# Kernel tuning notes

Hardware: AMD Instinct MI355X
Metric: run time of the kernel (lower is better)

The kernel has to match this reference:

```python
import jax, jax.numpy as jnp
import numpy as np

N_NODES = 50000
N_EDGES = 600000
D_EMB = 128
D_HID = 128
N_HEADS = 4
N_MABS = 7  # ISAB0(mab0,mab1), ISAB1(mab0,mab1), PMA, SAB, SAB
B, S = 16, 512
PROTO = 5


def setup_inputs() -> dict:
    key = jax.random.key(0)
    ks = jax.random.split(key, 24)
    nrm = lambda k, shape, s=0.05: jax.random.normal(k, shape, jnp.float32) * s
    node_embed = nrm(ks[0], (N_NODES + 1, D_EMB), 1.0).at[0].set(0.0)  # padding_idx=0
    return {
        'node_ids': jax.random.randint(ks[1], (B, S), 0, N_NODES),
        'edge_idx': jax.random.randint(ks[2], (2, N_EDGES), 0, N_NODES),
        'edge_attr': jax.random.normal(ks[3], (N_EDGES,), jnp.float32),
        'node_embed': node_embed,
        'lin_W': nrm(ks[4], (D_EMB, D_HID)), 'lin_b': jnp.zeros((D_HID,), jnp.float32),
        'gat_W': nrm(ks[5], (D_HID, D_HID)),
        'gat_att_src': nrm(ks[6], (D_HID,)), 'gat_att_dst': nrm(ks[7], (D_HID,)),
        'gat_bias': jnp.zeros((D_HID,), jnp.float32),
        'mab_Wq': nrm(ks[8], (N_MABS, D_HID, D_HID)), 'mab_bq': jnp.zeros((N_MABS, D_HID), jnp.float32),
        'mab_Wk': nrm(ks[9], (N_MABS, D_HID, D_HID)), 'mab_bk': jnp.zeros((N_MABS, D_HID), jnp.float32),
        'mab_Wv': nrm(ks[10], (N_MABS, D_HID, D_HID)), 'mab_bv': jnp.zeros((N_MABS, D_HID), jnp.float32),
        'mab_Wo': nrm(ks[11], (N_MABS, D_HID, D_HID)), 'mab_bo': jnp.zeros((N_MABS, D_HID), jnp.float32),
        'isab_I': nrm(ks[12], (2, 1, D_HID), 1.0),   # 2 ISAB blocks, num_inds=1
        'pma_S': nrm(ks[13], (1, D_HID), 1.0),       # num_outputs=1 seed
        'dec_W': nrm(ks[14], (D_HID, D_HID)), 'dec_b': jnp.zeros((D_HID,), jnp.float32),
        'prototypes': nrm(ks[15], (1, PROTO, D_HID), 1.0),
    }


def mab(Q, K, Wq, bq, Wk, bk, Wv, bv, Wo, bo):
    # Set-transformer MAB, ln=False; residual uses projected Q; scale by sqrt(full dim)
    D = Q.shape[-1]
    h, d = N_HEADS, D // N_HEADS
    Qp = Q @ Wq + bq
    Kp = K @ Wk + bk
    Vp = K @ Wv + bv
    sh = lambda x: x.reshape(x.shape[0], x.shape[1], h, d).transpose(0, 2, 1, 3)
    A = jax.nn.softmax(jnp.einsum('bhqd,bhkd->bhqk', sh(Qp), sh(Kp)) / np.sqrt(D).astype(np.float32))
    O = sh(Qp) + jnp.einsum('bhqk,bhkd->bhqd', A, sh(Vp))
    O = O.transpose(0, 2, 1, 3).reshape(Q.shape[0], Q.shape[1], D)
    return O + jax.nn.relu(O @ Wo + bo)


def reference(node_ids, edge_idx, edge_attr, node_embed, lin_W, lin_b, gat_W,
              gat_att_src, gat_att_dst, gat_bias, mab_Wq, mab_bq, mab_Wk, mab_bk,
              mab_Wv, mab_bv, mab_Wo, mab_bo, isab_I, pma_S, dec_W, dec_b, prototypes):
    # embed all nodes then linear
    x = node_embed[jnp.arange(N_NODES)] @ lin_W + lin_b          # [N, H]
    # GATConv (1 head, negative_slope=0.2, add_self_loops=True; edge_attr unused)
    loops = jnp.arange(N_NODES)
    src = jnp.concatenate([edge_idx[0], loops])
    dst = jnp.concatenate([edge_idx[1], loops])
    xw = x @ gat_W                                               # [N, H]
    a_s = xw @ gat_att_src                                       # [N]
    a_d = xw @ gat_att_dst
    e = jax.nn.leaky_relu(a_s[src] + a_d[dst], 0.2)              # [E+N]
    m = jax.ops.segment_max(e, dst, num_segments=N_NODES)
    ex = jnp.exp(e - m[dst])
    den = jax.ops.segment_sum(ex, dst, num_segments=N_NODES)
    coef = ex / den[dst]
    x = jax.ops.segment_sum(coef[:, None] * xw[src], dst, num_segments=N_NODES) + gat_bias
    # gather per-sample node sets
    X = x[node_ids]                                              # [B, S, H]
    b = X.shape[0]
    def mb(i, Q, K):
        return mab(Q, K, mab_Wq[i], mab_bq[i], mab_Wk[i], mab_bk[i],
                   mab_Wv[i], mab_bv[i], mab_Wo[i], mab_bo[i])
    # encoder: 2 ISAB blocks (num_inds=1)
    for i in range(2):
        Hb = mb(2 * i, jnp.broadcast_to(isab_I[i][None], (b, 1, D_HID)), X)
        X = mb(2 * i + 1, X, Hb)
    # decoder: PMA -> SAB -> SAB -> Linear
    X = mb(4, jnp.broadcast_to(pma_S[None], (b, 1, D_HID)), X)
    X = mb(5, X, X)
    X = mb(6, X, X)
    X = X @ dec_W + dec_b                                        # [B, 1, H]
    proto = jnp.broadcast_to(prototypes, (b, PROTO, D_HID))
    return jnp.concatenate([X, proto], axis=1)                   # [B, 6, H]
```

## Files before the change

kernel.cpp:

```cpp
#include <hip/hip_runtime.h>
#include <math.h>

#define N_NODES 50000
#define N_EDGES 600000
#define BATCH 16
#define SEQ 512
#define NROWS (BATCH*SEQ)
#define N_ITEMS (N_EDGES + N_NODES)

#define OFF_X      0L
#define OFF_ACC    1048576L
#define OFF_X2     2097152L
#define OFF_AS     3145728L
#define OFF_AD     3195728L
#define OFF_WC     3245728L
#define OFF_BC     3262112L
#define OFF_QP     3262240L
#define OFF_WKH    3262624L
#define OFF_CKH    3264160L
#define OFF_VAS    3264176L
#define OFF_VAD    3264304L
#define OFF_BFIN   3264432L
#define OFF_CSD    3264560L
#define OFF_VPOD   3264564L
#define OFF_MASK   3266612L
#define OFF_DEG    (OFF_MASK + 50000L)
#define OFF_FILL   (OFF_DEG + 8192L)
#define OFF_CNT    (OFF_FILL + 8192L)
#define ZERO_BYTES ((50000L + 8192L + 8192L + 4L) * 4L)
#define OFF_MAP    (OFF_CNT + 4L)
#define OFF_INV    (OFF_MAP + 50000L)
#define OFF_ROWPTR (OFF_INV + 8192L)
#define OFF_COL    (OFF_ROWPTR + 8194L)

__global__ __launch_bounds__(256) void prep_kernel(
    const float* __restrict__ lin_W, const float* __restrict__ lin_b,
    const float* __restrict__ gat_W,
    const float* __restrict__ mab_Wq, const float* __restrict__ mab_bq,
    const float* __restrict__ isab_I, const float* __restrict__ pma_S,
    float* __restrict__ Wc, float* __restrict__ bc, float* __restrict__ qp)
{
    int t = blockIdx.x * 256 + threadIdx.x;
    if (t < 16384) {
        int i = t >> 7, j = t & 127;
        float s = 0.f;
        for (int k = 0; k < 128; ++k) s += lin_W[i*128 + k] * gat_W[k*128 + j];
        Wc[t] = s;
    } else if (t < 16512) {
        int j = t - 16384;
        float s = 0.f;
        for (int k = 0; k < 128; ++k) s += lin_b[k] * gat_W[k*128 + j];
        bc[j] = s;
    } else if (t < 16896) {
        int u = t - 16512;
        int m = u >> 7, c = u & 127;
        int mi = m * 2;
        const float* vec = (m == 0) ? isab_I : (m == 1 ? isab_I + 128 : pma_S);
        float s = mab_bq[mi*128 + c];
        for (int k = 0; k < 128; ++k) s += vec[k] * mab_Wq[mi*16384 + k*128 + c];
        qp[u] = s;
    }
}

__global__ __launch_bounds__(256) void prep2_kernel(
    const float* __restrict__ mab_Wk, const float* __restrict__ mab_bk,
    const float* __restrict__ qp, const float* __restrict__ Wc,
    const float* __restrict__ bc, const float* __restrict__ att_src,
    const float* __restrict__ att_dst, const float* __restrict__ gat_bias,
    float* __restrict__ wkh, float* __restrict__ ckh,
    float* __restrict__ vas, float* __restrict__ vad,
    float* __restrict__ bfin, float* __restrict__ csd)
{
    int t = blockIdx.x * 256 + threadIdx.x;
    if (t < 1536) {
        int m = t >> 9;
        int h = (t >> 7) & 3;
        int j = t & 127;
        int mi = m * 2;
        const float* Wk = mab_Wk + mi*16384 + j*128 + h*32;
        const float* q  = qp + m*128 + h*32;
        float s = 0.f;
        #pragma unroll
        for (int d = 0; d < 32; ++d) s += Wk[d] * q[d];
        wkh[t] = s;
    } else if (t < 1548) {
        int u = t - 1536;
        int m = u >> 2, h = u & 3;
        int mi = m * 2;
        const float* bk = mab_bk + mi*128 + h*32;
        const float* q  = qp + m*128 + h*32;
        float s = 0.f;
        #pragma unroll
        for (int d = 0; d < 32; ++d) s += bk[d] * q[d];
        ckh[u] = s;
    } else if (t < 1676) {
        int k = t - 1548;
        float s = 0.f;
        for (int j = 0; j < 128; ++j) s += Wc[k*128 + j] * att_src[j];
        vas[k] = s;
    } else if (t < 1804) {
        int k = t - 1676;
        float s = 0.f;
        for (int j = 0; j < 128; ++j) s += Wc[k*128 + j] * att_dst[j];
        vad[k] = s;
    } else if (t < 1932) {
        int j = t - 1804;
        bfin[j] = bc[j] + gat_bias[j];
    } else if (t == 1932) {
        float s = 0.f;
        for (int j = 0; j < 128; ++j) s += bc[j] * att_src[j];
        csd[0] = s;
    } else if (t == 1933) {
        float s = 0.f;
        for (int j = 0; j < 128; ++j) s += bc[j] * att_dst[j];
        csd[1] = s;
    }
}

__global__ __launch_bounds__(256) void gemm0_kernel(
    const float* __restrict__ Xin, const float* __restrict__ W1,
    const float* __restrict__ b1, float* __restrict__ out1)
{
    __shared__ float Xs[16][128];
    int t = threadIdx.x;
    long row0 = (long)blockIdx.x * 16;
    #pragma unroll
    for (int i = 0; i < 8; ++i) {
        int idx = i*256 + t;
        int r = idx >> 7, k = idx & 127;
        Xs[r][k] = Xin[(row0 + r)*128 + k];
    }
    __syncthreads();
    int c  = t & 127;
    int hh = t >> 7;
    float acc1[8];
    #pragma unroll
    for (int r = 0; r < 8; ++r) acc1[r] = 0.f;
    for (int k4 = 0; k4 < 128; k4 += 4) {
        float xv[8][4];
        #pragma unroll
        for (int r = 0; r < 8; ++r) {
            float4 tmp = *(const float4*)&Xs[hh*8 + r][k4];
            xv[r][0] = tmp.x; xv[r][1] = tmp.y; xv[r][2] = tmp.z; xv[r][3] = tmp.w;
        }
        #pragma unroll
        for (int kk = 0; kk < 4; ++kk) {
            float w1 = W1[(k4 + kk)*128 + c];
            #pragma unroll
            for (int r = 0; r < 8; ++r) acc1[r] += xv[r][kk] * w1;
        }
    }
    float bb = b1[c];
    #pragma unroll
    for (int r = 0; r < 8; ++r) out1[(row0 + hh*8 + r)*128 + c] = acc1[r] + bb;
}

__global__ __launch_bounds__(256) void gemm_odd_kernel(
    const float* __restrict__ X, const float* __restrict__ Wq,
    const float* __restrict__ bq, const float* __restrict__ vpod,
    const float* __restrict__ Wo, const float* __restrict__ bo,
    float* __restrict__ Xout)
{
    __shared__ float Xs[16][128];
    __shared__ float O1[16][128];
    int t = threadIdx.x;
    long row0 = (long)blockIdx.x * 16;
    int bidx = (int)(row0 >> 9);
    #pragma unroll
    for (int i = 0; i < 8; ++i) {
        int idx = i*256 + t;
        int r = idx >> 7, k = idx & 127;
        Xs[r][k] = X[(row0 + r)*128 + k];
    }
    __syncthreads();
    int c  = t & 127;
    int hh = t >> 7;
    float acc[8];
    #pragma unroll
    for (int r = 0; r < 8; ++r) acc[r] = 0.f;
    for (int k4 = 0; k4 < 128; k4 += 4) {
        float xv[8][4];
        #pragma unroll
        for (int r = 0; r < 8; ++r) {
            float4 tmp = *(const float4*)&Xs[hh*8 + r][k4];
            xv[r][0] = tmp.x; xv[r][1] = tmp.y; xv[r][2] = tmp.z; xv[r][3] = tmp.w;
        }
        #pragma unroll
        for (int kk = 0; kk < 4; ++kk) {
            float w = Wq[(k4 + kk)*128 + c];
            #pragma unroll
            for (int r = 0; r < 8; ++r) acc[r] += xv[r][kk] * w;
        }
    }
    float bb = bq[c] + vpod[bidx*128 + c];
    #pragma unroll
    for (int r = 0; r < 8; ++r) O1[hh*8 + r][c] = acc[r] + bb;
    __syncthreads();
    #pragma unroll
    for (int r = 0; r < 8; ++r) acc[r] = 0.f;
    for (int k4 = 0; k4 < 128; k4 += 4) {
        float xv[8][4];
        #pragma unroll
        for (int r = 0; r < 8; ++r) {
            float4 tmp = *(const float4*)&O1[hh*8 + r][k4];
            xv[r][0] = tmp.x; xv[r][1] = tmp.y; xv[r][2] = tmp.z; xv[r][3] = tmp.w;
        }
        #pragma unroll
        for (int kk = 0; kk < 4; ++kk) {
            float w = Wo[(k4 + kk)*128 + c];
            #pragma unroll
            for (int r = 0; r < 8; ++r) acc[r] += xv[r][kk] * w;
        }
    }
    float bb2 = bo[c];
    #pragma unroll
    for (int r = 0; r < 8; ++r)
        Xout[(row0 + hh*8 + r)*128 + c] = O1[hh*8 + r][c] + fmaxf(acc[r] + bb2, 0.f);
}

__global__ __launch_bounds__(256) void avec_kernel(
    const float* __restrict__ embed, const float* __restrict__ vas,
    const float* __restrict__ vad, const float* __restrict__ csd,
    float* __restrict__ a_s, float* __restrict__ a_d)
{
    int w = threadIdx.x >> 6, lane = threadIdx.x & 63;
    long row = (long)blockIdx.x * 4 + w;
    const float* xr = embed + row*128 + lane*2;
    float x0 = xr[0], x1 = xr[1];
    float s = x0*vas[lane*2] + x1*vas[lane*2 + 1];
    float d = x0*vad[lane*2] + x1*vad[lane*2 + 1];
    #pragma unroll
    for (int off = 32; off > 0; off >>= 1) {
        s += __shfl_down(s, off);
        d += __shfl_down(d, off);
    }
    if (lane == 0) { a_s[row] = s + csd[0]; a_d[row] = d + csd[1]; }
}

__global__ void maskset_kernel(const int* __restrict__ node_ids, int* __restrict__ mask)
{
    int i = blockIdx.x*256 + threadIdx.x;
    if (i < NROWS) mask[node_ids[i]] = 1;
}

__global__ __launch_bounds__(256) void assign_kernel(
    const int* __restrict__ mask, int* __restrict__ map,
    int* __restrict__ inv, int* __restrict__ counter)
{
    __shared__ int wbase[4];
    int i = blockIdx.x*256 + threadIdx.x;
    bool act = (i < N_NODES) && mask[i];
    unsigned long long m = __ballot(act);
    int lane = threadIdx.x & 63;
    int w = threadIdx.x >> 6;
    if (lane == 0) wbase[w] = __popcll(m);
    __syncthreads();
    if (threadIdx.x == 0) {
        int tot = wbase[0] + wbase[1] + wbase[2] + wbase[3];
        int base = atomicAdd(counter, tot);
        int r = base;
        #pragma unroll
        for (int j = 0; j < 4; ++j) { int cj = wbase[j]; wbase[j] = r; r += cj; }
    }
    __syncthreads();
    if (i < N_NODES) {
        int c = -1;
        if (act) {
            c = wbase[w] + __popcll(m & ((1ull << lane) - 1ull));
            inv[c] = i;
        }
        map[i] = c;
    }
}

__global__ __launch_bounds__(256) void pass1_kernel(
    const int* __restrict__ edge_idx, const int* __restrict__ map,
    int* __restrict__ deg)
{
    int i = blockIdx.x*256 + threadIdx.x;
    if (i >= N_ITEMS) return;
    int dd = (i < N_EDGES) ? edge_idx[N_EDGES + i] : i - N_EDGES;
    int c = map[dd];
    if (c >= 0) atomicAdd(&deg[c], 1);
}

__global__ __launch_bounds__(256) void scan_kernel(const int* __restrict__ deg,
                                                   int* __restrict__ rowptr)
{
    __shared__ int part[256];
    __shared__ int pref[256];
    int t = threadIdx.x;
    int base = t * 32;
    int s = 0;
    #pragma unroll
    for (int j = 0; j < 32; ++j) s += deg[base + j];
    part[t] = s;
    __syncthreads();
    if (t == 0) {
        int run = 0;
        for (int i = 0; i < 256; ++i) { pref[i] = run; run += part[i]; }
    }
    __syncthreads();
    int run = pref[t];
    #pragma unroll
    for (int j = 0; j < 32; ++j) { rowptr[base + j] = run; run += deg[base + j]; }
    if (t == 255) rowptr[8192] = run;
}

__global__ __launch_bounds__(256) void pass2_kernel(
    const int* __restrict__ edge_idx, const int* __restrict__ map,
    const int* __restrict__ rowptr, int* __restrict__ fill,
    int* __restrict__ colx)
{
    int i = blockIdx.x*256 + threadIdx.x;
    if (i >= N_ITEMS) return;
    int s, dd;
    if (i < N_EDGES) { s = edge_idx[i]; dd = edge_idx[N_EDGES + i]; }
    else             { s = dd = i - N_EDGES; }
    int c = map[dd];
    if (c < 0) return;
    int pos = rowptr[c] + atomicAdd(&fill[c], 1);
    colx[pos] = s;
}

__global__ __launch_bounds__(256) void agg_kernel(
    const int* __restrict__ rowptr, const int* __restrict__ colx,
    const int* __restrict__ inv, const int* __restrict__ cnt,
    const float* __restrict__ a_s, const float* __restrict__ a_d,
    const float* __restrict__ embed, float* __restrict__ acc)
{
    int c = blockIdx.x*4 + (threadIdx.x >> 6);
    int lane = threadIdx.x & 63;
    if (c >= *cnt) return;
    int dd = inv[c];
    float ad = a_d[dd];
    int beg = rowptr[c], end = rowptr[c + 1];
    float s0 = 0.f, s1 = 0.f, den = 0.f;
    for (int j = beg; j < end; ++j) {
        int s = colx[j];
        float e = a_s[s] + ad;
        e = (e > 0.f) ? e : 0.2f * e;
        float ex = __expf(e);
        den += ex;
        float2 v = *(const float2*)(embed + (long)s*128 + lane*2);
        s0 += ex * v.x;
        s1 += ex * v.y;
    }
    float inv_d = 1.f / den;
    float* o = acc + (long)c*128 + lane*2;
    o[0] = s0 * inv_d;
    o[1] = s1 * inv_d;
}

__global__ __launch_bounds__(256) void gather_kernel(
    const int* __restrict__ node_ids, const int* __restrict__ map,
    const float* __restrict__ X2, float* __restrict__ X)
{
    int w = threadIdx.x >> 6, lane = threadIdx.x & 63;
    int j = blockIdx.x*4 + w;
    int c = map[node_ids[j]];
    const float2 v = *(const float2*)(X2 + (long)c*128 + lane*2);
    *(float2*)(X + (long)j*128 + lane*2) = v;
}

__device__ __forceinline__ float matvec_qs(
    const float* __restrict__ W, const float* xs, float (*red)[128], int t)
{
    int c = t & 127, q = t >> 7;
    float acc = 0.f;
    #pragma unroll
    for (int j = 0; j < 32; ++j) {
        int k = q*32 + j;
        acc += xs[k] * W[k*128 + c];
    }
    red[q][c] = acc;
    __syncthreads();
    float s = 0.f;
    if (t < 128) s = red[0][t] + red[1][t] + red[2][t] + red[3][t];
    __syncthreads();
    return s;
}

__global__ __launch_bounds__(512) void attn_even_kernel(
    const float* __restrict__ X, const float* __restrict__ qp,
    const float* __restrict__ wkh, const float* __restrict__ ckh,
    const float* __restrict__ Wv, const float* __restrict__ bv,
    const float* __restrict__ Wo, const float* __restrict__ bo,
    const float* __restrict__ Wv1, const float* __restrict__ bv1,
    float* __restrict__ vpod)
{
    __shared__ float l_sm[4][512];
    __shared__ float part[4][4][128];
    __shared__ float wks[4][128];
    __shared__ float u_sm[4][128];
    __shared__ float red[4][128];
    __shared__ float red64[4][64];
    __shared__ float mx[4], dn[4];
    __shared__ float qs[128], Ovec[128], Hsm[128];
    int b = blockIdx.x, t = threadIdx.x;
    if (t < 128) qs[t] = qp[t];
    wks[t >> 7][t & 127] = wkh[t];
    __syncthreads();
    const float scale = 0.088388347648318447f;
    float ck0 = ckh[0], ck1 = ckh[1], ck2 = ckh[2], ck3 = ckh[3];
    {
        const float* xr = X + ((long)b*512 + t)*128;
        float l[4] = {0.f, 0.f, 0.f, 0.f};
        for (int d4 = 0; d4 < 128; d4 += 4) {
            float4 xv = *(const float4*)&xr[d4];
            #pragma unroll
            for (int h = 0; h < 4; ++h)
                l[h] += xv.x*wks[h][d4] + xv.y*wks[h][d4+1]
                      + xv.z*wks[h][d4+2] + xv.w*wks[h][d4+3];
        }
        l_sm[0][t] = (l[0] + ck0) * scale;
        l_sm[1][t] = (l[1] + ck1) * scale;
        l_sm[2][t] = (l[2] + ck2) * scale;
        l_sm[3][t] = (l[3] + ck3) * scale;
    }
    __syncthreads();
    if (t < 256) {
        int h = t >> 6, i = t & 63;
        float m = -1e30f;
        #pragma unroll
        for (int j = 0; j < 8; ++j) m = fmaxf(m, l_sm[h][i + 64*j]);
        red64[h][i] = m;
    }
    __syncthreads();
    if (t < 4) {
        float m = -1e30f;
        for (int i = 0; i < 64; ++i) m = fmaxf(m, red64[t][i]);
        mx[t] = m;
    }
    __syncthreads();
    #pragma unroll
    for (int h = 0; h < 4; ++h) l_sm[h][t] = __expf(l_sm[h][t] - mx[h]);
    __syncthreads();
    if (t < 256) {
        int h = t >> 6, i = t & 63;
        float ssum = 0.f;
        #pragma unroll
        for (int j = 0; j < 8; ++j) ssum += l_sm[h][i + 64*j];
        red64[h][i] = ssum;
    }
    __syncthreads();
    if (t < 4) {
        float sm = 0.f;
        for (int i = 0; i < 64; ++i) sm += red64[t][i];
        dn[t] = 1.f / sm;
    }
    __syncthreads();
    {
        int q4 = t >> 7, d = t & 127;
        float a0 = 0.f, a1 = 0.f, a2 = 0.f, a3 = 0.f;
        const float* xc = X + ((long)b*512 + q4*128)*128 + d;
        for (int kk = 0; kk < 128; ++kk) {
            float xv = xc[(long)kk*128];
            int k = q4*128 + kk;
            a0 += xv * l_sm[0][k];
            a1 += xv * l_sm[1][k];
            a2 += xv * l_sm[2][k];
            a3 += xv * l_sm[3][k];
        }
        part[q4][0][d] = a0; part[q4][1][d] = a1; part[q4][2][d] = a2; part[q4][3][d] = a3;
    }
    __syncthreads();
    {
        int h = t >> 7, d = t & 127;
        u_sm[h][d] = (part[0][h][d] + part[1][h][d] + part[2][h][d] + part[3][h][d]) * dn[h];
    }
    __syncthreads();
    {
        int q4 = t >> 7, c = t & 127, h = c >> 5;
        float a = 0.f;
        #pragma unroll
        for (int j = 0; j < 32; ++j) {
            int k = q4*32 + j;
            a += u_sm[h][k] * Wv[k*128 + c];
        }
        red[q4][c] = a;
    }
    __syncthreads();
    if (t < 128) Ovec[t] = qs[t] + red[0][t] + red[1][t] + red[2][t] + red[3][t] + bv[t];
    __syncthreads();
    float mv = matvec_qs(Wo, Ovec, red, t);
    if (t < 128) Hsm[t] = Ovec[t] + fmaxf(mv + bo[t], 0.f);
    __syncthreads();
    float mv2 = matvec_qs(Wv1, Hsm, red, t);
    if (t < 128) vpod[b*128 + t] = mv2 + bv1[t];
}

__global__ __launch_bounds__(512) void attn_pma_kernel(
    const float* __restrict__ X, const float* __restrict__ qp,
    const float* __restrict__ wkh, const float* __restrict__ ckh,
    const float* __restrict__ mab_Wq, const float* __restrict__ mab_bq,
    const float* __restrict__ mab_Wv, const float* __restrict__ mab_bv,
    const float* __restrict__ mab_Wo, const float* __restrict__ mab_bo,
    const float* __restrict__ dec_W, const float* __restrict__ dec_b,
    const float* __restrict__ protos, float* __restrict__ out)
{
    __shared__ float l_sm[4][512];
    __shared__ float part[4][4][128];
    __shared__ float wks[4][128];
    __shared__ float u_sm[4][128];
    __shared__ float red[4][128];
    __shared__ float red64[4][64];
    __shared__ float mx[4], dn[4];
    __shared__ float qs[128], Ovec[128], S1[128], S2[128];
    int b = blockIdx.x, t = threadIdx.x;
    if (t < 128) qs[t] = qp[t];
    wks[t >> 7][t & 127] = wkh[t];
    __syncthreads();
    const float scale = 0.088388347648318447f;
    float ck0 = ckh[0], ck1 = ckh[1], ck2 = ckh[2], ck3 = ckh[3];
    {
        const float* xr = X + ((long)b*512 + t)*128;
        float l[4] = {0.f, 0.f, 0.f, 0.f};
        for (int d4 = 0; d4 < 128; d4 += 4) {
            float4 xv = *(const float4*)&xr[d4];
            #pragma unroll
            for (int h = 0; h < 4; ++h)
                l[h] += xv.x*wks[h][d4] + xv.y*wks[h][d4+1]
                      + xv.z*wks[h][d4+2] + xv.w*wks[h][d4+3];
        }
        l_sm[0][t] = (l[0] + ck0) * scale;
        l_sm[1][t] = (l[1] + ck1) * scale;
        l_sm[2][t] = (l[2] + ck2) * scale;
        l_sm[3][t] = (l[3] + ck3) * scale;
    }
    __syncthreads();
    if (t < 256) {
        int h = t >> 6, i = t & 63;
        float m = -1e30f;
        #pragma unroll
        for (int j = 0; j < 8; ++j) m = fmaxf(m, l_sm[h][i + 64*j]);
        red64[h][i] = m;
    }
    __syncthreads();
    if (t < 4) {
        float m = -1e30f;
        for (int i = 0; i < 64; ++i) m = fmaxf(m, red64[t][i]);
        mx[t] = m;
    }
    __syncthreads();
    #pragma unroll
    for (int h = 0; h < 4; ++h) l_sm[h][t] = __expf(l_sm[h][t] - mx[h]);
    __syncthreads();
    if (t < 256) {
        int h = t >> 6, i = t & 63;
        float ssum = 0.f;
        #pragma unroll
        for (int j = 0; j < 8; ++j) ssum += l_sm[h][i + 64*j];
        red64[h][i] = ssum;
    }
    __syncthreads();
    if (t < 4) {
        float sm = 0.f;
        for (int i = 0; i < 64; ++i) sm += red64[t][i];
        dn[t] = 1.f / sm;
    }
    __syncthreads();
    {
        int q4 = t >> 7, d = t & 127;
        float a0 = 0.f, a1 = 0.f, a2 = 0.f, a3 = 0.f;
        const float* xc = X + ((long)b*512 + q4*128)*128 + d;
        for (int kk = 0; kk < 128; ++kk) {
            float xv = xc[(long)kk*128];
            int k = q4*128 + kk;
            a0 += xv * l_sm[0][k];
            a1 += xv * l_sm[1][k];
            a2 += xv * l_sm[2][k];
            a3 += xv * l_sm[3][k];
        }
        part[q4][0][d] = a0; part[q4][1][d] = a1; part[q4][2][d] = a2; part[q4][3][d] = a3;
    }
    __syncthreads();
    {
        int h = t >> 7, d = t & 127;
        u_sm[h][d] = (part[0][h][d] + part[1][h][d] + part[2][h][d] + part[3][h][d]) * dn[h];
    }
    __syncthreads();
    {
        int q4 = t >> 7, c = t & 127, h = c >> 5;
        float a = 0.f;
        #pragma unroll
        for (int j = 0; j < 32; ++j) {
            int k = q4*32 + j;
            a += u_sm[h][k] * (mab_Wv + 4*16384)[k*128 + c];
        }
        red[q4][c] = a;
    }
    __syncthreads();
    if (t < 128) Ovec[t] = qs[t] + red[0][t] + red[1][t] + red[2][t] + red[3][t]
                         + mab_bv[4*128 + t];
    __syncthreads();
    float mv = matvec_qs(mab_Wo + 4*16384, Ovec, red, t);
    if (t < 128) S1[t] = Ovec[t] + fmaxf(mv + mab_bo[4*128 + t], 0.f);
    __syncthreads();
    float q5 = matvec_qs(mab_Wq + 5*16384, S1, red, t);
    float v5 = matvec_qs(mab_Wv + 5*16384, S1, red, t);
    if (t < 128) S2[t] = q5 + mab_bq[5*128 + t] + v5 + mab_bv[5*128 + t];
    __syncthreads();
    float m5 = matvec_qs(mab_Wo + 5*16384, S2, red, t);
    if (t < 128) S1[t] = S2[t] + fmaxf(m5 + mab_bo[5*128 + t], 0.f);
    __syncthreads();
    float q6 = matvec_qs(mab_Wq + 6*16384, S1, red, t);
    float v6 = matvec_qs(mab_Wv + 6*16384, S1, red, t);
    if (t < 128) S2[t] = q6 + mab_bq[6*128 + t] + v6 + mab_bv[6*128 + t];
    __syncthreads();
    float m6 = matvec_qs(mab_Wo + 6*16384, S2, red, t);
    if (t < 128) S1[t] = S2[t] + fmaxf(m6 + mab_bo[6*128 + t], 0.f);
    __syncthreads();
    float y = matvec_qs(dec_W, S1, red, t);
    if (t < 128) out[b*768 + t] = y + dec_b[t];
    {
        int p = t >> 7, c = t & 127;
        out[b*768 + (1 + p)*128 + c] = protos[p*128 + c];
        if (t < 128) out[b*768 + 640 + t] = protos[512 + t];
    }
}

extern "C" void kernel_launch(void* const* d_in, const int* in_sizes, int n_in,
                              void* d_out, int out_size, void* d_ws, size_t ws_size,
                              hipStream_t stream)
{
    (void)in_sizes; (void)n_in; (void)out_size; (void)ws_size;
    const int*   node_ids  = (const int*)d_in[0];
    const int*   edge_idx  = (const int*)d_in[1];
    const float* node_embed= (const float*)d_in[3];
    const float* lin_W     = (const float*)d_in[4];
    const float* lin_b     = (const float*)d_in[5];
    const float* gat_W     = (const float*)d_in[6];
    const float* att_src   = (const float*)d_in[7];
    const float* att_dst   = (const float*)d_in[8];
    const float* gat_bias  = (const float*)d_in[9];
    const float* mab_Wq    = (const float*)d_in[10];
    const float* mab_bq    = (const float*)d_in[11];
    const float* mab_Wk    = (const float*)d_in[12];
    const float* mab_bk    = (const float*)d_in[13];
    const float* mab_Wv    = (const float*)d_in[14];
    const float* mab_bv    = (const float*)d_in[15];
    const float* mab_Wo    = (const float*)d_in[16];
    const float* mab_bo    = (const float*)d_in[17];
    const float* isab_I    = (const float*)d_in[18];
    const float* pma_S     = (const float*)d_in[19];
    const float* dec_W     = (const float*)d_in[20];
    const float* dec_b     = (const float*)d_in[21];
    const float* protos    = (const float*)d_in[22];

    float* ws    = (float*)d_ws;
    float* X     = ws + OFF_X;
    float* acc   = ws + OFF_ACC;
    float* X2    = ws + OFF_X2;
    float* a_s   = ws + OFF_AS;
    float* a_d   = ws + OFF_AD;
    float* Wc    = ws + OFF_WC;
    float* bc    = ws + OFF_BC;
    float* qp    = ws + OFF_QP;
    float* wkh   = ws + OFF_WKH;
    float* ckh   = ws + OFF_CKH;
    float* vas   = ws + OFF_VAS;
    float* vad   = ws + OFF_VAD;
    float* bfin  = ws + OFF_BFIN;
    float* csd   = ws + OFF_CSD;
    float* vpod  = ws + OFF_VPOD;
    int*   mask  = (int*)(ws + OFF_MASK);
    int*   deg   = (int*)(ws + OFF_DEG);
    int*   fill  = (int*)(ws + OFF_FILL);
    int*   cnt   = (int*)(ws + OFF_CNT);
    int*   map   = (int*)(ws + OFF_MAP);
    int*   inv   = (int*)(ws + OFF_INV);
    int*   rowp  = (int*)(ws + OFF_ROWPTR);
    int*   colx  = (int*)(ws + OFF_COL);
    float* out   = (float*)d_out;

    hipMemsetAsync(ws + OFF_MASK, 0, ZERO_BYTES, stream);

    prep_kernel<<<66, 256, 0, stream>>>(lin_W, lin_b, gat_W, mab_Wq, mab_bq, isab_I, pma_S,
                                        Wc, bc, qp);
    prep2_kernel<<<8, 256, 0, stream>>>(mab_Wk, mab_bk, qp, Wc, bc, att_src, att_dst, gat_bias,
                                        wkh, ckh, vas, vad, bfin, csd);
    avec_kernel<<<N_NODES/4, 256, 0, stream>>>(node_embed, vas, vad, csd, a_s, a_d);
    maskset_kernel<<<(NROWS + 255)/256, 256, 0, stream>>>(node_ids, mask);
    assign_kernel<<<(N_NODES + 255)/256, 256, 0, stream>>>(mask, map, inv, cnt);
    pass1_kernel<<<(N_ITEMS + 255)/256, 256, 0, stream>>>(edge_idx, map, deg);
    scan_kernel<<<1, 256, 0, stream>>>(deg, rowp);
    pass2_kernel<<<(N_ITEMS + 255)/256, 256, 0, stream>>>(edge_idx, map, rowp, fill, colx);
    agg_kernel<<<NROWS/4, 256, 0, stream>>>(rowp, colx, inv, cnt, a_s, a_d, node_embed, acc);
    gemm0_kernel<<<NROWS/16, 256, 0, stream>>>(acc, Wc, bfin, X2);
    gather_kernel<<<NROWS/4, 256, 0, stream>>>(node_ids, map, X2, X);

    for (int i = 0; i < 2; ++i) {
        int o = 2*i + 1;
        attn_even_kernel<<<16, 512, 0, stream>>>(X, qp + i*128, wkh + i*512, ckh + i*4,
                                                 mab_Wv + (2*i)*16384, mab_bv + (2*i)*128,
                                                 mab_Wo + (2*i)*16384, mab_bo + (2*i)*128,
                                                 mab_Wv + o*16384, mab_bv + o*128,
                                                 vpod);
        gemm_odd_kernel<<<NROWS/16, 256, 0, stream>>>(X, mab_Wq + o*16384, mab_bq + o*128,
                                                      vpod, mab_Wo + o*16384, mab_bo + o*128,
                                                      X);
    }
    attn_pma_kernel<<<16, 512, 0, stream>>>(X, qp + 256, wkh + 1024, ckh + 8,
                                            mab_Wq, mab_bq, mab_Wv, mab_bv, mab_Wo, mab_bo,
                                            dec_W, dec_b, protos, out);
}
```

Measured before the change: 290.5 us.

## Run dense 128x128 GEMMs on MFMA with split-bf16 (bf16x3) precision

Replaces the scalar fp32 FMA GEMM kernels (the GAT linear and the fused odd-MAB Wq/Wo pair) with MFMA 16x16x32 bf16 kernels. Each fp32 operand is split into high and low bf16 parts and three products are accumulated, to keep close to fp32 accuracy. Weights are pre-packed into an MFMA fragment layout by a new pack kernel, which also absorbs the old prep2 work. The mask-setting kernel is folded into avec_kernel to save a launch. The cost is extra packing work, three MFMAs per tile and a small precision risk from the bf16x3 approximation.

```diff
diff --git a/kernel.cpp b/kernel.cpp
--- a/kernel.cpp
+++ b/kernel.cpp
@@ -23,7 +23,9 @@
 #define OFF_BFIN   3264432L
 #define OFF_CSD    3264560L
 #define OFF_VPOD   3264564L
-#define OFF_MASK   3266612L
+#define OFF_PWH    3266612L
+#define OFF_PWL    3307572L
+#define OFF_MASK   3348532L
 #define OFF_DEG    (OFF_MASK + 50000L)
 #define OFF_FILL   (OFF_DEG + 8192L)
 #define OFF_CNT    (OFF_FILL + 8192L)
@@ -32,6 +34,19 @@
 #define OFF_INV    (OFF_MAP + 50000L)
 #define OFF_ROWPTR (OFF_INV + 8192L)
 #define OFF_COL    (OFF_ROWPTR + 8194L)
+
+typedef __attribute__((ext_vector_type(8))) short bf16x8;
+typedef __attribute__((ext_vector_type(4))) float f32x4;
+#define MFMA16(a,b,c) __builtin_amdgcn_mfma_f32_16x16x32_bf16(a,b,c,0,0,0)
+
+__device__ __forceinline__ unsigned short f2bf_rne(float f) {
+    unsigned int u = __float_as_uint(f);
+    unsigned int r = u + 0x7FFFu + ((u >> 16) & 1u);
+    return (unsigned short)(r >> 16);
+}
+__device__ __forceinline__ float bf2f(unsigned short h) {
+    return __uint_as_float(((unsigned int)h) << 16);
+}
 
 __global__ __launch_bounds__(256) void prep_kernel(
     const float* __restrict__ lin_W, const float* __restrict__ lin_b,
@@ -62,167 +77,199 @@
     }
 }
 
-__global__ __launch_bounds__(256) void prep2_kernel(
+__global__ __launch_bounds__(256) void pack2_kernel(
+    const float* __restrict__ Wc, const float* __restrict__ bc,
+    const float* __restrict__ qp,
+    const float* __restrict__ mab_Wq, const float* __restrict__ mab_Wo,
     const float* __restrict__ mab_Wk, const float* __restrict__ mab_bk,
-    const float* __restrict__ qp, const float* __restrict__ Wc,
-    const float* __restrict__ bc, const float* __restrict__ att_src,
-    const float* __restrict__ att_dst, const float* __restrict__ gat_bias,
+    const float* __restrict__ att_src, const float* __restrict__ att_dst,
+    const float* __restrict__ gat_bias,
+    unsigned short* __restrict__ pWh, unsigned short* __restrict__ pWl,
     float* __restrict__ wkh, float* __restrict__ ckh,
     float* __restrict__ vas, float* __restrict__ vad,
     float* __restrict__ bfin, float* __restrict__ csd)
 {
-    int t = blockIdx.x * 256 + threadIdx.x;
-    if (t < 1536) {
-        int m = t >> 9;
-        int h = (t >> 7) & 3;
-        int j = t & 127;
-        int mi = m * 2;
-        const float* Wk = mab_Wk + mi*16384 + j*128 + h*32;
-        const float* q  = qp + m*128 + h*32;
-        float s = 0.f;
-        #pragma unroll
-        for (int d = 0; d < 32; ++d) s += Wk[d] * q[d];
-        wkh[t] = s;
-    } else if (t < 1548) {
-        int u = t - 1536;
-        int m = u >> 2, h = u & 3;
-        int mi = m * 2;
-        const float* bk = mab_bk + mi*128 + h*32;
-        const float* q  = qp + m*128 + h*32;
-        float s = 0.f;
-        #pragma unroll
-        for (int d = 0; d < 32; ++d) s += bk[d] * q[d];
-        ckh[u] = s;
-    } else if (t < 1676) {
-        int k = t - 1548;
-        float s = 0.f;
-        for (int j = 0; j < 128; ++j) s += Wc[k*128 + j] * att_src[j];
-        vas[k] = s;
-    } else if (t < 1804) {
-        int k = t - 1676;
-        float s = 0.f;
-        for (int j = 0; j < 128; ++j) s += Wc[k*128 + j] * att_dst[j];
-        vad[k] = s;
-    } else if (t < 1932) {
-        int j = t - 1804;
-        bfin[j] = bc[j] + gat_bias[j];
-    } else if (t == 1932) {
-        float s = 0.f;
-        for (int j = 0; j < 128; ++j) s += bc[j] * att_src[j];
-        csd[0] = s;
-    } else if (t == 1933) {
-        float s = 0.f;
-        for (int j = 0; j < 128; ++j) s += bc[j] * att_dst[j];
-        csd[1] = s;
-    }
-}
-
-__global__ __launch_bounds__(256) void gemm0_kernel(
-    const float* __restrict__ Xin, const float* __restrict__ W1,
-    const float* __restrict__ b1, float* __restrict__ out1)
-{
-    __shared__ float Xs[16][128];
+    int b = blockIdx.x, t = threadIdx.x;
+    if (b < 320) {
+        int tid = b*256 + t;
+        int m = tid >> 14;
+        int e = tid & 16383;
+        int j = e & 7, l = (e>>3) & 63, ct = (e>>9) & 7, kc = e >> 12;
+        int k = kc*32 + (l>>4)*8 + j;
+        int c = ct*16 + (l & 15);
+        const float* src;
+        if (m == 0) src = Wc;
+        else if (m == 1) src = mab_Wq + 1*16384;
+        else if (m == 2) src = mab_Wo + 1*16384;
+        else if (m == 3) src = mab_Wq + 3*16384;
+        else src = mab_Wo + 3*16384;
+        float v = src[k*128 + c];
+        unsigned short h = f2bf_rne(v);
+        pWh[tid] = h;
+        pWl[tid] = f2bf_rne(v - bf2f(h));
+    } else if (b == 320) {
+        for (int it = 0; it < 6; ++it) {
+            int u = it*256 + t;
+            int m = u >> 9, h = (u >> 7) & 3, j = u & 127;
+            const float* Wk = mab_Wk + (2*m)*16384 + j*128 + h*32;
+            const float* q  = qp + m*128 + h*32;
+            float s = 0.f;
+            #pragma unroll
+            for (int d = 0; d < 32; ++d) s += Wk[d] * q[d];
+            wkh[u] = s;
+        }
+        if (t < 12) {
+            int m = t >> 2, h = t & 3;
+            const float* bk = mab_bk + (2*m)*128 + h*32;
+            const float* q  = qp + m*128 + h*32;
+            float s = 0.f;
+            #pragma unroll
+            for (int d = 0; d < 32; ++d) s += bk[d] * q[d];
+            ckh[t] = s;
+        }
+    } else {
+        if (t < 128) {
+            float s = 0.f;
+            for (int j = 0; j < 128; ++j) s += Wc[t*128 + j] * att_src[j];
+            vas[t] = s;
+            bfin[t] = bc[t] + gat_bias[t];
+        } else {
+            int k = t - 128;
+            float s = 0.f;
+            for (int j = 0; j < 128; ++j) s += Wc[k*128 + j] * att_dst[j];
+            vad[k] = s;
+        }
+        if (t == 0) {
+            float s = 0.f;
+            for (int j = 0; j < 128; ++j) s += bc[j] * att_src[j];
+            csd[0] = s;
+        }
+        if (t == 1) {
+            float s = 0.f;
+            for (int j = 0; j < 128; ++j) s += bc[j] * att_dst[j];
+            csd[1] = s;
+        }
+    }
+}
+
+__device__ __forceinline__ void mfma_stage(
+    const float (*Xs)[132], int arow, int ao, int lane,
+    const unsigned short* __restrict__ pWh, const unsigned short* __restrict__ pWl,
+    f32x4 acc[8])
+{
+    #pragma unroll
+    for (int kc = 0; kc < 4; ++kc) {
+        float4 fa = *(const float4*)&Xs[arow][kc*32 + ao];
+        float4 fb = *(const float4*)&Xs[arow][kc*32 + ao + 4];
+        float f[8] = {fa.x, fa.y, fa.z, fa.w, fb.x, fb.y, fb.z, fb.w};
+        bf16x8 ah, al;
+        #pragma unroll
+        for (int j = 0; j < 8; ++j) {
+            unsigned short h = f2bf_rne(f[j]);
+            ah[j] = (short)h;
+            al[j] = (short)f2bf_rne(f[j] - bf2f(h));
+        }
+        #pragma unroll
+        for (int ct = 0; ct < 8; ++ct) {
+            int fo = ((kc*8 + ct)*64 + lane)*8;
+            bf16x8 bh = *(const bf16x8*)(pWh + fo);
+            bf16x8 bl = *(const bf16x8*)(pWl + fo);
+            acc[ct] = MFMA16(ah, bh, acc[ct]);
+            acc[ct] = MFMA16(ah, bl, acc[ct]);
+            acc[ct] = MFMA16(al, bh, acc[ct]);
+        }
+    }
+}
+
+__global__ __launch_bounds__(256) void mfma_lin_kernel(
+    const float* __restrict__ Xin,
+    const unsigned short* __restrict__ pWh, const unsigned short* __restrict__ pWl,
+    const float* __restrict__ b1, float* __restrict__ out)
+{
+    __shared__ float Xs[64][132];
     int t = threadIdx.x;
-    long row0 = (long)blockIdx.x * 16;
-    #pragma unroll
-    for (int i = 0; i < 8; ++i) {
+    long row0 = (long)blockIdx.x * 64;
+    #pragma unroll
+    for (int i = 0; i < 32; ++i) {
         int idx = i*256 + t;
         int r = idx >> 7, k = idx & 127;
         Xs[r][k] = Xin[(row0 + r)*128 + k];
     }
     __syncthreads();
-    int c  = t & 127;
-    int hh = t >> 7;
-    float acc1[8];
-    #pragma unroll
-    for (int r = 0; r < 8; ++r) acc1[r] = 0.f;
-    for (int k4 = 0; k4 < 128; k4 += 4) {
-        float xv[8][4];
-        #pragma unroll
-        for (int r = 0; r < 8; ++r) {
-            float4 tmp = *(const float4*)&Xs[hh*8 + r][k4];
-            xv[r][0] = tmp.x; xv[r][1] = tmp.y; xv[r][2] = tmp.z; xv[r][3] = tmp.w;
-        }
-        #pragma unroll
-        for (int kk = 0; kk < 4; ++kk) {
-            float w1 = W1[(k4 + kk)*128 + c];
-            #pragma unroll
-            for (int r = 0; r < 8; ++r) acc1[r] += xv[r][kk] * w1;
-        }
-    }
-    float bb = b1[c];
-    #pragma unroll
-    for (int r = 0; r < 8; ++r) out1[(row0 + hh*8 + r)*128 + c] = acc1[r] + bb;
-}
-
-__global__ __launch_bounds__(256) void gemm_odd_kernel(
-    const float* __restrict__ X, const float* __restrict__ Wq,
+    int lane = t & 63, wv = t >> 6;
+    int arow = wv*16 + (lane & 15), ao = (lane >> 4)*8;
+    int crow0 = wv*16 + (lane >> 4)*4, ccol = lane & 15;
+    f32x4 acc[8];
+    #pragma unroll
+    for (int ct = 0; ct < 8; ++ct) { acc[ct][0]=0.f; acc[ct][1]=0.f; acc[ct][2]=0.f; acc[ct][3]=0.f; }
+    mfma_stage(Xs, arow, ao, lane, pWh, pWl, acc);
+    #pragma unroll
+    for (int ct = 0; ct < 8; ++ct) {
+        int cc = ct*16 + ccol;
+        float bb = b1[cc];
+        #pragma unroll
+        for (int i = 0; i < 4; ++i)
+            out[(row0 + crow0 + i)*128 + cc] = acc[ct][i] + bb;
+    }
+}
+
+__global__ __launch_bounds__(256) void mfma_odd_kernel(
+    const float* __restrict__ Xin,
+    const unsigned short* __restrict__ pQh, const unsigned short* __restrict__ pQl,
     const float* __restrict__ bq, const float* __restrict__ vpod,
-    const float* __restrict__ Wo, const float* __restrict__ bo,
-    float* __restrict__ Xout)
-{
-    __shared__ float Xs[16][128];
-    __shared__ float O1[16][128];
+    const unsigned short* __restrict__ pOh, const unsigned short* __restrict__ pOl,
+    const float* __restrict__ bo, float* __restrict__ Xout)
+{
+    __shared__ float Xs[64][132];
     int t = threadIdx.x;
-    long row0 = (long)blockIdx.x * 16;
-    int bidx = (int)(row0 >> 9);
-    #pragma unroll
-    for (int i = 0; i < 8; ++i) {
+    long row0 = (long)blockIdx.x * 64;
+    #pragma unroll
+    for (int i = 0; i < 32; ++i) {
         int idx = i*256 + t;
         int r = idx >> 7, k = idx & 127;
-        Xs[r][k] = X[(row0 + r)*128 + k];
-    }
-    __syncthreads();
-    int c  = t & 127;
-    int hh = t >> 7;
-    float acc[8];
-    #pragma unroll
-    for (int r = 0; r < 8; ++r) acc[r] = 0.f;
-    for (int k4 = 0; k4 < 128; k4 += 4) {
-        float xv[8][4];
-        #pragma unroll
-        for (int r = 0; r < 8; ++r) {
-            float4 tmp = *(const float4*)&Xs[hh*8 + r][k4];
-            xv[r][0] = tmp.x; xv[r][1] = tmp.y; xv[r][2] = tmp.z; xv[r][3] = tmp.w;
-        }
-        #pragma unroll
-        for (int kk = 0; kk < 4; ++kk) {
-            float w = Wq[(k4 + kk)*128 + c];
-            #pragma unroll
-            for (int r = 0; r < 8; ++r) acc[r] += xv[r][kk] * w;
-        }
-    }
-    float bb = bq[c] + vpod[bidx*128 + c];
-    #pragma unroll
-    for (int r = 0; r < 8; ++r) O1[hh*8 + r][c] = acc[r] + bb;
-    __syncthreads();
-    #pragma unroll
-    for (int r = 0; r < 8; ++r) acc[r] = 0.f;
-    for (int k4 = 0; k4 < 128; k4 += 4) {
-        float xv[8][4];
-        #pragma unroll
-        for (int r = 0; r < 8; ++r) {
-            float4 tmp = *(const float4*)&O1[hh*8 + r][k4];
-            xv[r][0] = tmp.x; xv[r][1] = tmp.y; xv[r][2] = tmp.z; xv[r][3] = tmp.w;
-        }
-        #pragma unroll
-        for (int kk = 0; kk < 4; ++kk) {
-            float w = Wo[(k4 + kk)*128 + c];
-            #pragma unroll
-            for (int r = 0; r < 8; ++r) acc[r] += xv[r][kk] * w;
-        }
-    }
-    float bb2 = bo[c];
-    #pragma unroll
-    for (int r = 0; r < 8; ++r)
-        Xout[(row0 + hh*8 + r)*128 + c] = O1[hh*8 + r][c] + fmaxf(acc[r] + bb2, 0.f);
+        Xs[r][k] = Xin[(row0 + r)*128 + k];
+    }
+    __syncthreads();
+    int lane = t & 63, wv = t >> 6;
+    int arow = wv*16 + (lane & 15), ao = (lane >> 4)*8;
+    int crow0 = wv*16 + (lane >> 4)*4, ccol = lane & 15;
+    int bidx = (int)(row0 >> 9);
+    f32x4 acc[8];
+    #pragma unroll
+    for (int ct = 0; ct < 8; ++ct) { acc[ct][0]=0.f; acc[ct][1]=0.f; acc[ct][2]=0.f; acc[ct][3]=0.f; }
+    mfma_stage(Xs, arow, ao, lane, pQh, pQl, acc);
+    #pragma unroll
+    for (int ct = 0; ct < 8; ++ct) {
+        int cc = ct*16 + ccol;
+        float bb = bq[cc] + vpod[bidx*128 + cc];
+        #pragma unroll
+        for (int i = 0; i < 4; ++i) Xs[crow0 + i][cc] = acc[ct][i] + bb;
+    }
+    #pragma unroll
+    for (int ct = 0; ct < 8; ++ct) { acc[ct][0]=0.f; acc[ct][1]=0.f; acc[ct][2]=0.f; acc[ct][3]=0.f; }
+    mfma_stage(Xs, arow, ao, lane, pOh, pOl, acc);
+    #pragma unroll
+    for (int ct = 0; ct < 8; ++ct) {
+        int cc = ct*16 + ccol;
+        float bb = bo[cc];
+        #pragma unroll
+        for (int i = 0; i < 4; ++i) {
+            float o1 = Xs[crow0 + i][cc];
+            Xout[(row0 + crow0 + i)*128 + cc] = o1 + fmaxf(acc[ct][i] + bb, 0.f);
+        }
+    }
 }
 
 __global__ __launch_bounds__(256) void avec_kernel(
     const float* __restrict__ embed, const float* __restrict__ vas,
     const float* __restrict__ vad, const float* __restrict__ csd,
+    const int* __restrict__ node_ids, int* __restrict__ mask,
     float* __restrict__ a_s, float* __restrict__ a_d)
 {
+    if (blockIdx.x < 32) {
+        int idx = blockIdx.x*256 + threadIdx.x;
+        mask[node_ids[idx]] = 1;
+    }
     int w = threadIdx.x >> 6, lane = threadIdx.x & 63;
     long row = (long)blockIdx.x * 4 + w;
     const float* xr = embed + row*128 + lane*2;
@@ -235,12 +282,6 @@
         d += __shfl_down(d, off);
     }
     if (lane == 0) { a_s[row] = s + csd[0]; a_d[row] = d + csd[1]; }
-}
-
-__global__ void maskset_kernel(const int* __restrict__ node_ids, int* __restrict__ mask)
-{
-    int i = blockIdx.x*256 + threadIdx.x;
-    if (i < NROWS) mask[node_ids[i]] = 1;
 }
 
 __global__ __launch_bounds__(256) void assign_kernel(
@@ -664,6 +705,8 @@
     float* bfin  = ws + OFF_BFIN;
     float* csd   = ws + OFF_CSD;
     float* vpod  = ws + OFF_VPOD;
+    unsigned short* pWh = (unsigned short*)(ws + OFF_PWH);
+    unsigned short* pWl = (unsigned short*)(ws + OFF_PWL);
     int*   mask  = (int*)(ws + OFF_MASK);
     int*   deg   = (int*)(ws + OFF_DEG);
     int*   fill  = (int*)(ws + OFF_FILL);
@@ -678,16 +721,17 @@
 
     prep_kernel<<<66, 256, 0, stream>>>(lin_W, lin_b, gat_W, mab_Wq, mab_bq, isab_I, pma_S,
                                         Wc, bc, qp);
-    prep2_kernel<<<8, 256, 0, stream>>>(mab_Wk, mab_bk, qp, Wc, bc, att_src, att_dst, gat_bias,
-                                        wkh, ckh, vas, vad, bfin, csd);
-    avec_kernel<<<N_NODES/4, 256, 0, stream>>>(node_embed, vas, vad, csd, a_s, a_d);
-    maskset_kernel<<<(NROWS + 255)/256, 256, 0, stream>>>(node_ids, mask);
+    pack2_kernel<<<322, 256, 0, stream>>>(Wc, bc, qp, mab_Wq, mab_Wo, mab_Wk, mab_bk,
+                                          att_src, att_dst, gat_bias,
+                                          pWh, pWl, wkh, ckh, vas, vad, bfin, csd);
+    avec_kernel<<<N_NODES/4, 256, 0, stream>>>(node_embed, vas, vad, csd, node_ids, mask,
+                                               a_s, a_d);
     assign_kernel<<<(N_NODES + 255)/256, 256, 0, stream>>>(mask, map, inv, cnt);
     pass1_kernel<<<(N_ITEMS + 255)/256, 256, 0, stream>>>(edge_idx, map, deg);
     scan_kernel<<<1, 256, 0, stream>>>(deg, rowp);
     pass2_kernel<<<(N_ITEMS + 255)/256, 256, 0, stream>>>(edge_idx, map, rowp, fill, colx);
     agg_kernel<<<NROWS/4, 256, 0, stream>>>(rowp, colx, inv, cnt, a_s, a_d, node_embed, acc);
-    gemm0_kernel<<<NROWS/16, 256, 0, stream>>>(acc, Wc, bfin, X2);
+    mfma_lin_kernel<<<NROWS/64, 256, 0, stream>>>(acc, pWh, pWl, bfin, X2);
     gather_kernel<<<NROWS/4, 256, 0, stream>>>(node_ids, map, X2, X);
 
     for (int i = 0; i < 2; ++i) {
@@ -697,9 +741,13 @@
                                                  mab_Wo + (2*i)*16384, mab_bo + (2*i)*128,
                                                  mab_Wv + o*16384, mab_bv + o*128,
                                                  vpod);
-        gemm_odd_kernel<<<NROWS/16, 256, 0, stream>>>(X, mab_Wq + o*16384, mab_bq + o*128,
-                                                      vpod, mab_Wo + o*16384, mab_bo + o*128,
-                                                      X);
+        int mq = 1 + 2*i;
+        int mo = 2 + 2*i;
+        mfma_odd_kernel<<<NROWS/64, 256, 0, stream>>>(X,
+                                                      pWh + mq*16384, pWl + mq*16384,
+                                                      mab_bq + o*128, vpod,
+                                                      pWh + mo*16384, pWl + mo*16384,
+                                                      mab_bo + o*128, X);
     }
     attn_pma_kernel<<<16, 512, 0, stream>>>(X, qp + 256, wkh + 1024, ckh + 8,
                                             mab_Wq, mab_bq, mab_Wv, mab_bv, mab_Wo, mab_bo,
```

Measured after the change: 297.7 us. +2.5%, slower.
